# Kernel optimization log

Hardware: AMD Instinct MI355X
Metric: run time of the kernel (lower is better)

The kernel has to match this reference:

```python
import jax, jax.numpy as jnp
import numpy as np

DIM = 1024
HEADS = 16
DIM_HEAD = 64
INNER = HEADS * DIM_HEAD
SCALE = 8.0  # default scale in plain_cosine_sim_attention
EPS = 1e-5


def setup_inputs() -> dict:
    key = jax.random.key(0)
    ks = jax.random.split(key, 5)
    b, n = 2, 2048
    x = jax.random.normal(ks[0], (b, n, DIM), dtype=jnp.float32)
    ln_w = jnp.ones((DIM,), dtype=jnp.float32)
    ln_b = jnp.zeros((DIM,), dtype=jnp.float32)
    W_qkv = jax.random.normal(ks[1], (DIM, 3 * INNER), dtype=jnp.float32) * (DIM ** -0.5)
    W_out = jax.random.normal(ks[2], (INNER, DIM), dtype=jnp.float32) * (INNER ** -0.5)
    return {"x": x, "ln_w": ln_w, "ln_b": ln_b, "W_qkv": W_qkv, "W_out": W_out}


def _l2norm(t):
    return t / jnp.clip(jnp.linalg.norm(t, axis=-1, keepdims=True), 1e-12)


def reference(x, ln_w, ln_b, W_qkv, W_out):
    b, n, _ = x.shape
    # LayerNorm
    mu = jnp.mean(x, axis=-1, keepdims=True)
    var = jnp.var(x, axis=-1, keepdims=True)
    xn = (x - mu) * jax.lax.rsqrt(var + EPS) * ln_w + ln_b
    # QKV projection (no bias)
    qkv = xn @ W_qkv  # [b, n, 3*inner]
    q, k, v = jnp.split(qkv, 3, axis=-1)
    # [b, n, h*d] -> [b, h, n, d]
    def to_heads(t):
        return t.reshape(b, n, HEADS, DIM_HEAD).transpose(0, 2, 1, 3)
    q, k, v = to_heads(q), to_heads(k), to_heads(v)
    # cosine-sim attention: l2-normalize q, k then scaled dot product
    q = _l2norm(q)
    k = _l2norm(k)
    sim = jnp.einsum('bhid,bhjd->bhij', q, k) * SCALE
    # causal mask
    causal = jnp.tril(jnp.ones((n, n), dtype=bool))
    sim = jnp.where(causal, sim, jnp.finfo(sim.dtype).min)
    attn = jax.nn.softmax(sim, axis=-1)
    o = jnp.einsum('bhij,bhjd->bhid', attn, v)
    # [b, h, n, d] -> [b, n, h*d]
    o = o.transpose(0, 2, 1, 3).reshape(b, n, INNER)
    return o @ W_out
```

## Files before the change

### kernel.cpp

```cpp
#include <hip/hip_runtime.h>
#include <hip/hip_bf16.h>

typedef __attribute__((ext_vector_type(8))) short short8;
typedef __attribute__((ext_vector_type(4))) float floatx4;

__device__ __forceinline__ ushort f2bf(float f) {
    union { __hip_bfloat16 h; ushort u; } cv;
    cv.h = __float2bfloat16(f);
    return cv.u;
}
__device__ __forceinline__ float bf2f(ushort u) {
    union { ushort u; __hip_bfloat16 h; } cv;
    cv.u = u;
    return __bfloat162float(cv.h);
}
__device__ __forceinline__ ushort f2bf_rtz(float f) {
    union { float f; unsigned u; } cv;
    cv.f = f;
    return (ushort)(cv.u >> 16);
}

typedef __attribute__((address_space(1))) void* gas1_t;
typedef __attribute__((address_space(3))) void* las3_t;
__device__ __forceinline__ void cp16(const ushort* g, ushort* l) {
    __builtin_amdgcn_global_load_lds((gas1_t)(unsigned long long)g,
                                     (las3_t)(unsigned long long)l, 16, 0, 0);
}

__global__ __launch_bounds__(256) void transpose_cast(const float* __restrict__ in,
                                                      ushort* __restrict__ out,
                                                      int R, int C) {
    __shared__ float tile[32][33];
    int c0 = blockIdx.x * 32, r0 = blockIdx.y * 32;
    int tx = threadIdx.x, ty = threadIdx.y;
    for (int j = 0; j < 32; j += 8)
        tile[ty + j][tx] = in[(size_t)(r0 + ty + j) * C + c0 + tx];
    __syncthreads();
    for (int j = 0; j < 32; j += 8)
        out[(size_t)(c0 + ty + j) * R + r0 + tx] = f2bf(tile[tx][ty + j]);
}

__global__ __launch_bounds__(256) void ln_kernel(const float* __restrict__ x,
                                                 const float* __restrict__ lw,
                                                 const float* __restrict__ lb,
                                                 ushort* __restrict__ xn) {
    int row = blockIdx.x;
    int tid = threadIdx.x;
    const float4* xr = (const float4*)(x + (size_t)row * 1024);
    float4 v = xr[tid];
    float s = v.x + v.y + v.z + v.w;
    float sq = v.x * v.x + v.y * v.y + v.z * v.z + v.w * v.w;
    for (int off = 32; off; off >>= 1) {
        s += __shfl_xor(s, off);
        sq += __shfl_xor(sq, off);
    }
    __shared__ float ls[4], lq[4];
    int wave = tid >> 6, lane = tid & 63;
    if (lane == 0) { ls[wave] = s; lq[wave] = sq; }
    __syncthreads();
    s = ls[0] + ls[1] + ls[2] + ls[3];
    sq = lq[0] + lq[1] + lq[2] + lq[3];
    float mu = s * (1.0f / 1024.0f);
    float var = sq * (1.0f / 1024.0f) - mu * mu;
    float rs = rsqrtf(var + 1e-5f);
    const float4* wr = (const float4*)lw;
    const float4* br = (const float4*)lb;
    float4 wv = wr[tid], bv = br[tid];
    ushort4 o;
    o.x = f2bf((v.x - mu) * rs * wv.x + bv.x);
    o.y = f2bf((v.y - mu) * rs * wv.y + bv.y);
    o.z = f2bf((v.z - mu) * rs * wv.z + bv.z);
    o.w = f2bf((v.w - mu) * rs * wv.w + bv.w);
    *(ushort4*)&xn[(size_t)row * 1024 + tid * 4] = o;
}

template <typename OutT>
__global__ __launch_bounds__(256) void gemm_bt(const ushort* __restrict__ A,
                                               const ushort* __restrict__ Bt,
                                               OutT* __restrict__ C,
                                               int M, int N, int K) {
    __shared__ ushort As[2][128 * 32];
    __shared__ ushort Bs[2][128 * 32];
    const int tid = threadIdx.x;
    const int wave = tid >> 6, lane = tid & 63;
    const int quad = lane >> 4, l15 = lane & 15;
    const int wm = (wave >> 1) * 64, wn = (wave & 1) * 64;
    const int bm = blockIdx.y * 128, bn = blockIdx.x * 128;

    const int s0 = tid, s1 = tid + 256;
    const int row0 = s0 >> 2, src0 = (s0 & 3) ^ (row0 & 3);
    const int row1 = s1 >> 2, src1 = (s1 & 3) ^ (row1 & 3);

    floatx4 acc[4][4];
    floatx4 z4 = {0.f, 0.f, 0.f, 0.f};
    for (int mi = 0; mi < 4; mi++)
        for (int ni = 0; ni < 4; ni++) acc[mi][ni] = z4;

    const ushort* Ap0 = A + (size_t)(bm + row0) * K + src0 * 8;
    const ushort* Ap1 = A + (size_t)(bm + row1) * K + src1 * 8;
    const ushort* Bp0 = Bt + (size_t)(bn + row0) * K + src0 * 8;
    const ushort* Bp1 = Bt + (size_t)(bn + row1) * K + src1 * 8;

    const int T = K >> 5;
    cp16(Ap0, &As[0][wave * 512]);
    cp16(Ap1, &As[0][2048 + wave * 512]);
    cp16(Bp0, &Bs[0][wave * 512]);
    cp16(Bp1, &Bs[0][2048 + wave * 512]);

    for (int t = 0; t < T; t++) {
        __syncthreads();
        if (t + 1 < T) {
            const int nb = (t + 1) & 1;
            const int k0n = (t + 1) << 5;
            cp16(Ap0 + k0n, &As[nb][wave * 512]);
            cp16(Ap1 + k0n, &As[nb][2048 + wave * 512]);
            cp16(Bp0 + k0n, &Bs[nb][wave * 512]);
            cp16(Bp1 + k0n, &Bs[nb][2048 + wave * 512]);
        }
        const ushort* Ab = As[t & 1];
        const ushort* Bb = Bs[t & 1];
        short8 af[4], bfr[4];
        for (int mi = 0; mi < 4; mi++) {
            int ra = wm + mi * 16 + l15;
            af[mi] = *(const short8*)&Ab[ra * 32 + ((quad ^ (ra & 3)) << 3)];
        }
        for (int ni = 0; ni < 4; ni++) {
            int rb = wn + ni * 16 + l15;
            bfr[ni] = *(const short8*)&Bb[rb * 32 + ((quad ^ (rb & 3)) << 3)];
        }
        for (int mi = 0; mi < 4; mi++)
            for (int ni = 0; ni < 4; ni++)
                acc[mi][ni] = __builtin_amdgcn_mfma_f32_16x16x32_bf16(
                    af[mi], bfr[ni], acc[mi][ni], 0, 0, 0);
    }
    for (int mi = 0; mi < 4; mi++) {
        for (int ni = 0; ni < 4; ni++) {
            for (int r = 0; r < 4; r++) {
                int row = bm + wm + mi * 16 + quad * 4 + r;
                int col = bn + wn + ni * 16 + l15;
                float val = acc[mi][ni][r];
                if constexpr (sizeof(OutT) == 2)
                    ((ushort*)C)[(size_t)row * N + col] = f2bf(val);
                else
                    ((float*)C)[(size_t)row * N + col] = val;
            }
        }
    }
}

__global__ __launch_bounds__(256) void prep(const ushort* __restrict__ qkv,
                                            ushort* __restrict__ Qt,
                                            ushort* __restrict__ Kt,
                                            ushort* __restrict__ Vb) {
    const int nb = blockIdx.x;
    const int h = blockIdx.y;
    const int b = blockIdx.z;
    const int bh = b * 16 + h;
    const int tid = threadIdx.x, wave = tid >> 6, lane = tid & 63;
    __shared__ ushort vt[64][72];

    union S8 { short8 v; ushort u[8]; };
    for (int i = 0; i < 2; i++) {
        int c = tid + i * 256;
        int nl = c >> 3, sg = c & 7;
        S8 vv;
        vv.v = *(const short8*)&qkv[(size_t)(b * 2048 + nb * 64 + nl) * 3072 + 2048 + h * 64 + sg * 8];
        for (int j = 0; j < 8; j++) vt[sg * 8 + j][nl] = vv.u[j];
    }
    __syncthreads();
    for (int i = 0; i < 2; i++) {
        int c = tid + i * 256;
        int d = c >> 3, sg = c & 7;
        *(short8*)&Vb[((size_t)bh * 32 + nb) * 4096 + d * 64 + sg * 8] =
            *(const short8*)&vt[d][sg * 8];
    }

    for (int j = 0; j < 16; j++) {
        int nl = wave * 16 + j;
        size_t rowb = (size_t)(b * 2048 + nb * 64 + nl) * 3072 + h * 64;
        size_t orow = ((size_t)bh * 2048 + nb * 64 + nl) * 64;

        float qv = bf2f(qkv[rowb + lane]);
        float ss = qv * qv;
        for (int off = 32; off; off >>= 1) ss += __shfl_xor(ss, off);
        float inv = 1.0f / fmaxf(sqrtf(ss), 1e-12f);
        Qt[orow + lane] = f2bf(qv * inv);

        float kv = bf2f(qkv[rowb + 1024 + lane]);
        ss = kv * kv;
        for (int off = 32; off; off >>= 1) ss += __shfl_xor(ss, off);
        inv = 1.0f / fmaxf(sqrtf(ss), 1e-12f);
        Kt[orow + lane] = f2bf(kv * inv);
    }
}

#define LOG2E8 11.541560327111707f

__global__ __launch_bounds__(256) void flash_attn(const ushort* __restrict__ Qt,
                                                  const ushort* __restrict__ Kt,
                                                  const ushort* __restrict__ Vb,
                                                  ushort* __restrict__ O) {
    const int id = blockIdx.x;
    const int xcd = id & 7, slot = id >> 3;
    const int bh = xcd * 4 + (slot >> 4);
    const int pairi = slot & 15;
    const int b = bh >> 4, h = bh & 15;
    const int tid = threadIdx.x;
    const int wave = tid >> 6, lane = tid & 63;
    const int quad = lane >> 4, l15 = lane & 15;

    __shared__ ushort Ks[2][64 * 64];
    __shared__ ushort Vs[2][64 * 64];
    __shared__ ushort Ps[4][16 * 72];

    const int ch0 = tid, ch1 = tid + 256;
    const int r0 = ch0 >> 3, sg0 = (ch0 & 7) ^ (r0 & 7);
    const int r1 = ch1 >> 3, sg1 = (ch1 & 7) ^ (r1 & 7);

    const ushort* Kp0 = Kt + ((size_t)bh * 2048 + r0) * 64 + sg0 * 8;
    const ushort* Kp1 = Kt + ((size_t)bh * 2048 + r1) * 64 + sg1 * 8;
    const ushort* Vp0 = Vb + (size_t)bh * 131072 + r0 * 64 + sg0 * 8;
    const ushort* Vp1 = Vb + (size_t)bh * 131072 + r1 * 64 + sg1 * 8;

    floatx4 z4 = {0.f, 0.f, 0.f, 0.f};

    for (int pass = 0; pass < 2; pass++) {
        const int st = pass ? (31 - pairi) : pairi;
        const int q0 = st * 64;

        const ushort* Qp = Qt + ((size_t)bh * 2048 + q0 + wave * 16 + l15) * 64;
        short8 qf0 = *(const short8*)(Qp + quad * 8);
        short8 qf1 = *(const short8*)(Qp + 32 + quad * 8);

        float rs_acc[4] = {0.f, 0.f, 0.f, 0.f};
        floatx4 o_acc[4];
        for (int ni = 0; ni < 4; ni++) o_acc[ni] = z4;

        __syncthreads();
        cp16(Kp0, &Ks[0][wave * 512]);
        cp16(Kp1, &Ks[0][2048 + wave * 512]);
        cp16(Vp0, &Vs[0][wave * 512]);
        cp16(Vp1, &Vs[0][2048 + wave * 512]);

        for (int kt = 0; kt <= st; kt++) {
            __syncthreads();
            if (kt < st) {
                const int nb2 = (kt + 1) & 1;
                const size_t to = (size_t)(kt + 1) * 4096;
                cp16(Kp0 + to, &Ks[nb2][wave * 512]);
                cp16(Kp1 + to, &Ks[nb2][2048 + wave * 512]);
                cp16(Vp0 + to, &Vs[nb2][wave * 512]);
                cp16(Vp1 + to, &Vs[nb2][2048 + wave * 512]);
            }
            const ushort* Kb = Ks[kt & 1];
            const ushort* Vb_ = Vs[kt & 1];

            floatx4 s_acc[4];
            for (int ni = 0; ni < 4; ni++) s_acc[ni] = z4;
            for (int ni = 0; ni < 4; ni++) {
                int rb = ni * 16 + l15;
                short8 kf0 = *(const short8*)&Kb[rb * 64 + ((quad ^ (rb & 7)) << 3)];
                short8 kf1 = *(const short8*)&Kb[rb * 64 + (((quad + 4) ^ (rb & 7)) << 3)];
                s_acc[ni] = __builtin_amdgcn_mfma_f32_16x16x32_bf16(qf0, kf0, s_acc[ni], 0, 0, 0);
                s_acc[ni] = __builtin_amdgcn_mfma_f32_16x16x32_bf16(qf1, kf1, s_acc[ni], 0, 0, 0);
            }

            const bool diag = (kt == st);
            for (int ni = 0; ni < 4; ni++) {
                const int col_loc = ni * 16 + l15;
                for (int r = 0; r < 4; r++) {
                    float e = __builtin_amdgcn_exp2f(
                        fmaf(s_acc[ni][r], LOG2E8, -LOG2E8));
                    if (diag && col_loc > wave * 16 + quad * 4 + r) e = 0.f;
                    rs_acc[r] += e;
                    Ps[wave][(quad * 4 + r) * 72 + col_loc] = f2bf_rtz(e);
                }
            }

            short8 pa0 = *(const short8*)&Ps[wave][l15 * 72 + quad * 8];
            short8 pa1 = *(const short8*)&Ps[wave][l15 * 72 + 32 + quad * 8];
            for (int ni = 0; ni < 4; ni++) {
                int rv = ni * 16 + l15;
                short8 v0 = *(const short8*)&Vb_[rv * 64 + ((quad ^ (rv & 7)) << 3)];
                short8 v1 = *(const short8*)&Vb_[rv * 64 + (((quad + 4) ^ (rv & 7)) << 3)];
                o_acc[ni] = __builtin_amdgcn_mfma_f32_16x16x32_bf16(pa0, v0, o_acc[ni], 0, 0, 0);
                o_acc[ni] = __builtin_amdgcn_mfma_f32_16x16x32_bf16(pa1, v1, o_acc[ni], 0, 0, 0);
            }
        }

        for (int r = 0; r < 4; r++) {
            float rs = rs_acc[r];
            for (int off = 1; off < 16; off <<= 1) rs += __shfl_xor(rs, off);
            float inv = 1.0f / rs;
            int grow = q0 + wave * 16 + quad * 4 + r;
            size_t rowbase = ((size_t)b * 2048 + grow) * 1024 + h * 64;
            for (int ni = 0; ni < 4; ni++)
                O[rowbase + ni * 16 + l15] = f2bf(o_acc[ni][r] * inv);
        }
    }
}

extern "C" void kernel_launch(void* const* d_in, const int* in_sizes, int n_in,
                              void* d_out, int out_size, void* d_ws, size_t ws_size,
                              hipStream_t stream) {
    const float* x = (const float*)d_in[0];
    const float* ln_w = (const float*)d_in[1];
    const float* ln_b = (const float*)d_in[2];
    const float* W_qkv = (const float*)d_in[3];
    const float* W_out = (const float*)d_in[4];

    char* w = (char*)d_ws;
    ushort* xn    = (ushort*)(w);
    ushort* WqkvT = (ushort*)(w + (8ull << 20));
    ushort* WoutT = (ushort*)(w + (14ull << 20));
    ushort* qkv   = (ushort*)(w + (16ull << 20));
    ushort* Vb    = (ushort*)(w + (40ull << 20));
    ushort* Qt    = (ushort*)(w + (48ull << 20));
    ushort* obuf  = (ushort*)(w + (56ull << 20));
    ushort* Kt    = (ushort*)(w + (64ull << 20));

    transpose_cast<<<dim3(96, 32), dim3(32, 8), 0, stream>>>(W_qkv, WqkvT, 1024, 3072);
    transpose_cast<<<dim3(32, 32), dim3(32, 8), 0, stream>>>(W_out, WoutT, 1024, 1024);
    ln_kernel<<<4096, 256, 0, stream>>>(x, ln_w, ln_b, xn);
    gemm_bt<ushort><<<dim3(24, 32), 256, 0, stream>>>(xn, WqkvT, qkv, 4096, 3072, 1024);
    prep<<<dim3(32, 16, 2), 256, 0, stream>>>(qkv, Qt, Kt, Vb);
    flash_attn<<<512, 256, 0, stream>>>(Qt, Kt, Vb, obuf);
    gemm_bt<float><<<dim3(8, 32), 256, 0, stream>>>(obuf, WoutT, (float*)d_out, 4096, 1024, 1024);
}
```

Measured before the change: 196.3 us.

## Fuse QKV l2norm and V transpose into GEMM epilogue, merge weight transposes

```diff
diff --git a/kernel.cpp b/kernel.cpp
--- a/kernel.cpp
+++ b/kernel.cpp
@@ -27,11 +27,16 @@
                                      (las3_t)(unsigned long long)l, 16, 0, 0);
 }
 
-__global__ __launch_bounds__(256) void transpose_cast(const float* __restrict__ in,
-                                                      ushort* __restrict__ out,
-                                                      int R, int C) {
+__global__ __launch_bounds__(256) void transpose_cast2(const float* __restrict__ Wqkv,
+                                                       const float* __restrict__ Wout,
+                                                       ushort* __restrict__ WqkvT,
+                                                       ushort* __restrict__ WoutT) {
     __shared__ float tile[32][33];
-    int c0 = blockIdx.x * 32, r0 = blockIdx.y * 32;
+    int bx = blockIdx.x, by = blockIdx.y;
+    const float* in; ushort* out; int R = 1024, C;
+    if (bx < 96) { in = Wqkv; out = WqkvT; C = 3072; }
+    else { in = Wout; out = WoutT; C = 1024; bx -= 96; }
+    int c0 = bx * 32, r0 = by * 32;
     int tx = threadIdx.x, ty = threadIdx.y;
     for (int j = 0; j < 32; j += 8)
         tile[ty + j][tx] = in[(size_t)(r0 + ty + j) * C + c0 + tx];
@@ -74,11 +79,113 @@
     *(ushort4*)&xn[(size_t)row * 1024 + tid * 4] = o;
 }
 
-template <typename OutT>
-__global__ __launch_bounds__(256) void gemm_bt(const ushort* __restrict__ A,
-                                               const ushort* __restrict__ Bt,
-                                               OutT* __restrict__ C,
-                                               int M, int N, int K) {
+__global__ __launch_bounds__(256) void gemm_qkv_fused(const ushort* __restrict__ A,
+                                                      const ushort* __restrict__ Bt,
+                                                      ushort* __restrict__ Qt,
+                                                      ushort* __restrict__ Kt,
+                                                      ushort* __restrict__ Vb) {
+    __shared__ ushort smem[18432];
+    const int K = 1024, T = 32;
+    const int tid = threadIdx.x;
+    const int wave = tid >> 6, lane = tid & 63;
+    const int quad = lane >> 4, l15 = lane & 15;
+    const int wm = (wave >> 1) * 64, wn = (wave & 1) * 64;
+    const int bm = blockIdx.y * 128, bn = blockIdx.x;
+
+    const int s0 = tid, s1 = tid + 256;
+    const int row0 = s0 >> 2, src0 = (s0 & 3) ^ (row0 & 3);
+    const int row1 = s1 >> 2, src1 = (s1 & 3) ^ (row1 & 3);
+
+    floatx4 acc[4][4];
+    floatx4 z4 = {0.f, 0.f, 0.f, 0.f};
+    for (int mi = 0; mi < 4; mi++)
+        for (int ni = 0; ni < 4; ni++) acc[mi][ni] = z4;
+
+    const ushort* Ap0 = A + (size_t)(bm + row0) * K + src0 * 8;
+    const ushort* Ap1 = A + (size_t)(bm + row1) * K + src1 * 8;
+    const ushort* Bp0 = Bt + (size_t)(bn * 128 + row0) * K + src0 * 8;
+    const ushort* Bp1 = Bt + (size_t)(bn * 128 + row1) * K + src1 * 8;
+
+    ushort* As = smem;
+    ushort* Bs = smem + 8192;
+
+    cp16(Ap0, &As[wave * 512]);
+    cp16(Ap1, &As[2048 + wave * 512]);
+    cp16(Bp0, &Bs[wave * 512]);
+    cp16(Bp1, &Bs[2048 + wave * 512]);
+
+    for (int t = 0; t < T; t++) {
+        __syncthreads();
+        if (t + 1 < T) {
+            const int nb = (t + 1) & 1;
+            const int k0n = (t + 1) << 5;
+            cp16(Ap0 + k0n, &As[nb * 4096 + wave * 512]);
+            cp16(Ap1 + k0n, &As[nb * 4096 + 2048 + wave * 512]);
+            cp16(Bp0 + k0n, &Bs[nb * 4096 + wave * 512]);
+            cp16(Bp1 + k0n, &Bs[nb * 4096 + 2048 + wave * 512]);
+        }
+        const ushort* Ab = As + (t & 1) * 4096;
+        const ushort* Bb = Bs + (t & 1) * 4096;
+        short8 af[4], bfr[4];
+        for (int mi = 0; mi < 4; mi++) {
+            int ra = wm + mi * 16 + l15;
+            af[mi] = *(const short8*)&Ab[ra * 32 + ((quad ^ (ra & 3)) << 3)];
+        }
+        for (int ni = 0; ni < 4; ni++) {
+            int rb = wn + ni * 16 + l15;
+            bfr[ni] = *(const short8*)&Bb[rb * 32 + ((quad ^ (rb & 3)) << 3)];
+        }
+        for (int mi = 0; mi < 4; mi++)
+            for (int ni = 0; ni < 4; ni++)
+                acc[mi][ni] = __builtin_amdgcn_mfma_f32_16x16x32_bf16(
+                    af[mi], bfr[ni], acc[mi][ni], 0, 0, 0);
+    }
+
+    const int col_base = bn * 128 + wn;
+    const int type = col_base >> 10;
+    const int h = (col_base & 1023) >> 6;
+    const int row_base = bm + wm;
+
+    if (type < 2) {
+        ushort* dst = (type == 0) ? Qt : Kt;
+        for (int mi = 0; mi < 4; mi++) {
+            for (int r = 0; r < 4; r++) {
+                float ss = 0.f;
+                for (int ni = 0; ni < 4; ni++) ss += acc[mi][ni][r] * acc[mi][ni][r];
+                for (int off = 1; off < 16; off <<= 1) ss += __shfl_xor(ss, off);
+                float inv = rsqrtf(fmaxf(ss, 1e-24f));
+                int rg = row_base + mi * 16 + quad * 4 + r;
+                int bb = rg >> 11, n = rg & 2047;
+                size_t orow = ((size_t)(bb * 16 + h) * 2048 + n) * 64;
+                for (int ni = 0; ni < 4; ni++)
+                    dst[orow + ni * 16 + l15] = f2bf(acc[mi][ni][r] * inv);
+            }
+        }
+    } else {
+        __syncthreads();
+        ushort* tr = smem + wave * 4608;
+        for (int mi = 0; mi < 4; mi++)
+            for (int ni = 0; ni < 4; ni++)
+                for (int r = 0; r < 4; r++) {
+                    int row_l = mi * 16 + quad * 4 + r;
+                    int col_l = ni * 16 + l15;
+                    tr[col_l * 72 + row_l] = f2bf(acc[mi][ni][r]);
+                }
+        int bb = row_base >> 11, n0 = row_base & 2047;
+        size_t vbase = ((size_t)(bb * 16 + h) * 32 + (n0 >> 6)) * 4096;
+        const int dl = lane >> 3, nc = (lane & 7) * 8;
+        for (int i = 0; i < 8; i++) {
+            int d = dl + i * 8;
+            short8 val = *(const short8*)&tr[d * 72 + nc];
+            *(short8*)&Vb[vbase + (size_t)d * 64 + nc] = val;
+        }
+    }
+}
+
+__global__ __launch_bounds__(256) void gemm_out(const ushort* __restrict__ A,
+                                                const ushort* __restrict__ Bt,
+                                                float* __restrict__ C,
+                                                int M, int N, int K) {
     __shared__ ushort As[2][128 * 32];
     __shared__ ushort Bs[2][128 * 32];
     const int tid = threadIdx.x;
@@ -133,65 +240,13 @@
                 acc[mi][ni] = __builtin_amdgcn_mfma_f32_16x16x32_bf16(
                     af[mi], bfr[ni], acc[mi][ni], 0, 0, 0);
     }
-    for (int mi = 0; mi < 4; mi++) {
-        for (int ni = 0; ni < 4; ni++) {
+    for (int mi = 0; mi < 4; mi++)
+        for (int ni = 0; ni < 4; ni++)
             for (int r = 0; r < 4; r++) {
                 int row = bm + wm + mi * 16 + quad * 4 + r;
                 int col = bn + wn + ni * 16 + l15;
-                float val = acc[mi][ni][r];
-                if constexpr (sizeof(OutT) == 2)
-                    ((ushort*)C)[(size_t)row * N + col] = f2bf(val);
-                else
-                    ((float*)C)[(size_t)row * N + col] = val;
-            }
-        }
-    }
-}
-
-__global__ __launch_bounds__(256) void prep(const ushort* __restrict__ qkv,
-                                            ushort* __restrict__ Qt,
-                                            ushort* __restrict__ Kt,
-                                            ushort* __restrict__ Vb) {
-    const int nb = blockIdx.x;
-    const int h = blockIdx.y;
-    const int b = blockIdx.z;
-    const int bh = b * 16 + h;
-    const int tid = threadIdx.x, wave = tid >> 6, lane = tid & 63;
-    __shared__ ushort vt[64][72];
-
-    union S8 { short8 v; ushort u[8]; };
-    for (int i = 0; i < 2; i++) {
-        int c = tid + i * 256;
-        int nl = c >> 3, sg = c & 7;
-        S8 vv;
-        vv.v = *(const short8*)&qkv[(size_t)(b * 2048 + nb * 64 + nl) * 3072 + 2048 + h * 64 + sg * 8];
-        for (int j = 0; j < 8; j++) vt[sg * 8 + j][nl] = vv.u[j];
-    }
-    __syncthreads();
-    for (int i = 0; i < 2; i++) {
-        int c = tid + i * 256;
-        int d = c >> 3, sg = c & 7;
-        *(short8*)&Vb[((size_t)bh * 32 + nb) * 4096 + d * 64 + sg * 8] =
-            *(const short8*)&vt[d][sg * 8];
-    }
-
-    for (int j = 0; j < 16; j++) {
-        int nl = wave * 16 + j;
-        size_t rowb = (size_t)(b * 2048 + nb * 64 + nl) * 3072 + h * 64;
-        size_t orow = ((size_t)bh * 2048 + nb * 64 + nl) * 64;
-
-        float qv = bf2f(qkv[rowb + lane]);
-        float ss = qv * qv;
-        for (int off = 32; off; off >>= 1) ss += __shfl_xor(ss, off);
-        float inv = 1.0f / fmaxf(sqrtf(ss), 1e-12f);
-        Qt[orow + lane] = f2bf(qv * inv);
-
-        float kv = bf2f(qkv[rowb + 1024 + lane]);
-        ss = kv * kv;
-        for (int off = 32; off; off >>= 1) ss += __shfl_xor(ss, off);
-        inv = 1.0f / fmaxf(sqrtf(ss), 1e-12f);
-        Kt[orow + lane] = f2bf(kv * inv);
-    }
+                C[(size_t)row * N + col] = acc[mi][ni][r];
+            }
 }
 
 #define LOG2E8 11.541560327111707f
@@ -313,17 +368,14 @@
     ushort* xn    = (ushort*)(w);
     ushort* WqkvT = (ushort*)(w + (8ull << 20));
     ushort* WoutT = (ushort*)(w + (14ull << 20));
-    ushort* qkv   = (ushort*)(w + (16ull << 20));
-    ushort* Vb    = (ushort*)(w + (40ull << 20));
-    ushort* Qt    = (ushort*)(w + (48ull << 20));
-    ushort* obuf  = (ushort*)(w + (56ull << 20));
-    ushort* Kt    = (ushort*)(w + (64ull << 20));
-
-    transpose_cast<<<dim3(96, 32), dim3(32, 8), 0, stream>>>(W_qkv, WqkvT, 1024, 3072);
-    transpose_cast<<<dim3(32, 32), dim3(32, 8), 0, stream>>>(W_out, WoutT, 1024, 1024);
+    ushort* Vb    = (ushort*)(w + (16ull << 20));
+    ushort* Qt    = (ushort*)(w + (24ull << 20));
+    ushort* Kt    = (ushort*)(w + (32ull << 20));
+    ushort* obuf  = (ushort*)(w + (40ull << 20));
+
+    transpose_cast2<<<dim3(128, 32), dim3(32, 8), 0, stream>>>(W_qkv, W_out, WqkvT, WoutT);
     ln_kernel<<<4096, 256, 0, stream>>>(x, ln_w, ln_b, xn);
-    gemm_bt<ushort><<<dim3(24, 32), 256, 0, stream>>>(xn, WqkvT, qkv, 4096, 3072, 1024);
-    prep<<<dim3(32, 16, 2), 256, 0, stream>>>(qkv, Qt, Kt, Vb);
+    gemm_qkv_fused<<<dim3(24, 32), 256, 0, stream>>>(xn, WqkvT, Qt, Kt, Vb);
     flash_attn<<<512, 256, 0, stream>>>(Qt, Kt, Vb, obuf);
-    gemm_bt<float><<<dim3(8, 32), 256, 0, stream>>>(obuf, WoutT, (float*)d_out, 4096, 1024, 1024);
-}
+    gemm_out<<<dim3(8, 32), 256, 0, stream>>>(obuf, WoutT, (float*)d_out, 4096, 1024, 1024);
+}
```

Result: faster. 179.4 us (-8.6%).
